# Kernel optimization log

Measured on AMD Instinct MI355X. Metric: run time of the kernel, lower is better.

Reference implementation:

```python
import jax, jax.numpy as jnp
import numpy as np

EPS = 1e-5
NEG_SLOPE = 0.2

def _layernorm(x, g, b):
    mu = x.mean(-1, keepdims=True)
    var = ((x - mu) ** 2).mean(-1, keepdims=True)
    return (x - mu) * jax.lax.rsqrt(var + EPS) * g + b

def _forward(h, edge_attr, rel_emb, W_l, b_l, W_r, b_r, W_e, att, bias, gate,
             g1, bt1, g2, bt2, Wf1, bf1, Wf2, bf2, edge_index, edge_type):
    N, F = h.shape
    R, H, C = att.shape
    HC = H * C
    E = edge_type.shape[0]
    De = edge_attr.shape[1]
    src, dst = edge_index[0], edge_index[1]

    # per-relation GATv2 linear projections: lin_l / lin_r  -> [N, R, H*C]
    xl = jnp.einsum('nf,rfh->nrh', h, W_l) + b_l
    xr = jnp.einsum('nf,rfh->nrh', h, W_r) + b_r
    # gather per edge using its own relation's weights
    xl_e = xl[src, edge_type]          # [E, HC]  (source, lin_l)
    xr_e = xr[dst, edge_type]          # [E, HC]  (dest,  lin_r)

    # edge features: lin_edge over concat([edge_attr, rel_emb[r]]) with per-relation weights
    e_feat = jnp.zeros((E, HC), dtype=h.dtype)
    for r in range(R):
        vr = edge_attr @ W_e[r, :De] + rel_emb[r] @ W_e[r, De:]  # [E,HC] + [HC]
        e_feat = jnp.where((edge_type == r)[:, None], vr, e_feat)

    # GATv2 attention score
    x = jax.nn.leaky_relu(xl_e + xr_e + e_feat, NEG_SLOPE).reshape(E, H, C)
    score = jnp.einsum('ehc,ehc->eh', x, att[edge_type])  # [E, H]

    # segment softmax per (destination node, relation)
    seg = dst * R + edge_type                              # [E]
    m = jax.lax.stop_gradient(jax.ops.segment_max(score, seg, num_segments=N * R))
    alpha = jnp.exp(score - m[seg])
    denom = jax.ops.segment_sum(alpha, seg, num_segments=N * R)
    alpha = alpha / denom[seg]                             # [E, H]

    # aggregate messages alpha * x_j (x_j = lin_l source features)
    msg = (xl_e.reshape(E, H, C) * alpha[..., None]).reshape(E, HC)
    agg = jax.ops.segment_sum(msg, seg, num_segments=N * R).reshape(N, R, H, C)
    h_rel = agg.mean(axis=2) + bias                        # concat=False -> head mean; [N, R, C]

    # learnable gated fusion over relations
    gw = jax.nn.softmax(gate)
    h_msg = jnp.einsum('r,nrc->nc', gw, h_rel)

    h1 = _layernorm(h + h_msg, g1, bt1)
    ffn = jax.nn.silu(h1 @ Wf1 + bf1) @ Wf2 + bf2
    return _layernorm(h1 + ffn, g2, bt2)


def setup_inputs() -> dict:
    key = jax.random.key(0)
    ks = jax.random.split(key, 16)
    N, F, E, De, Dr, R, H = 40000, 128, 150000, 16, 8, 4, 4
    C = F; HC = H * C; FFN = int(F * 2.0)
    s = 0.05
    return {
        'h': jax.random.normal(ks[0], (N, F), jnp.float32),
        'edge_index': jax.random.randint(ks[1], (2, E), 0, N),
        'edge_attr': jax.random.normal(ks[2], (E, De), jnp.float32),
        'edge_type': jax.random.randint(ks[3], (E,), 0, R),
        'rel_emb': jax.random.normal(ks[4], (R, Dr), jnp.float32) * s,
        'W_l': jax.random.normal(ks[5], (R, F, HC), jnp.float32) * s,
        'b_l': jnp.zeros((R, HC), jnp.float32),
        'W_r': jax.random.normal(ks[6], (R, F, HC), jnp.float32) * s,
        'b_r': jnp.zeros((R, HC), jnp.float32),
        'W_e': jax.random.normal(ks[7], (R, De + Dr, HC), jnp.float32) * s,
        'att': jax.random.normal(ks[8], (R, H, C), jnp.float32) * s,
        'bias': jnp.zeros((R, C), jnp.float32),
        'gate': jax.random.normal(ks[9], (R,), jnp.float32) * 0.5,
        'g1': jnp.ones((F,), jnp.float32), 'bt1': jnp.zeros((F,), jnp.float32),
        'g2': jnp.ones((F,), jnp.float32), 'bt2': jnp.zeros((F,), jnp.float32),
        'Wf1': jax.random.normal(ks[10], (F, FFN), jnp.float32) * s,
        'bf1': jnp.zeros((FFN,), jnp.float32),
        'Wf2': jax.random.normal(ks[11], (FFN, F), jnp.float32) * s,
        'bf2': jnp.zeros((F,), jnp.float32),
    }


def reference(h, edge_index, edge_attr, edge_type, rel_emb, W_l, b_l, W_r, b_r,
              W_e, att, bias, gate, g1, bt1, g2, bt2, Wf1, bf1, Wf2, bf2):
    return _forward(h, edge_attr, rel_emb, W_l, b_l, W_r, b_r, W_e, att, bias, gate,
                    g1, bt1, g2, bt2, Wf1, bf1, Wf2, bf2, edge_index, edge_type)
```

## Files before the change

kernel.cpp:

```cpp
#include <hip/hip_runtime.h>
#include <hip/hip_bf16.h>

#define NF   128
#define HCC  512
#define FFND 256
#define NEG  0.2f
#define EPSLN 1e-5f

typedef __attribute__((ext_vector_type(8))) short short8;
typedef __attribute__((ext_vector_type(4))) float f32x4;

__global__ void init_gw_kernel(const float* __restrict__ gate, float* __restrict__ gw) {
  if (threadIdx.x == 0 && blockIdx.x == 0) {
    float a = gate[0], b = gate[1], c = gate[2], d = gate[3];
    float m = fmaxf(fmaxf(a, b), fmaxf(c, d));
    float e0 = __expf(a - m), e1 = __expf(b - m), e2 = __expf(c - m), e3 = __expf(d - m);
    float s = e0 + e1 + e2 + e3;
    gw[0] = e0 / s; gw[1] = e1 / s; gw[2] = e2 / s; gw[3] = e3 / s;
  }
}

__global__ void init_all_kernel(float* __restrict__ denom, int* __restrict__ sorted,
                                int ndenom, int nsorted) {
  int i = blockIdx.x * 256 + threadIdx.x;
  if (i < ndenom)  denom[i] = 0.f;
  if (i < nsorted) sorted[i] = -1;
}

__global__ void init_hmsg_kernel(const float* __restrict__ gw, const float* __restrict__ bias,
                                 float* __restrict__ hmsg, int total) {
  int i = blockIdx.x * 256 + threadIdx.x;
  if (i < total) {
    int c = i & 127;
    hmsg[i] = gw[0]*bias[c] + gw[1]*bias[128+c] + gw[2]*bias[256+c] + gw[3]*bias[384+c];
  }
}

__global__ void transpose_bf16_kernel(const float* __restrict__ in, __hip_bfloat16* __restrict__ out,
                                      int rows, int cols, int total) {
  int i = blockIdx.x * 256 + threadIdx.x;
  if (i >= total) return;
  int per = rows * cols;
  int b = i / per, rem = i % per;
  int rr = rem / cols, cc = rem % cols;
  out[(size_t)b * per + (size_t)cc * rows + rr] = __float2bfloat16(in[i]);
}

__global__ void cvt_bf16_kernel(const float* __restrict__ in, __hip_bfloat16* __restrict__ out, int n) {
  int i4 = (blockIdx.x * 256 + threadIdx.x) * 4;
  if (i4 >= n) return;
  float4 v = *(const float4*)(in + i4);
  out[i4]     = __float2bfloat16(v.x);
  out[i4 + 1] = __float2bfloat16(v.y);
  out[i4 + 2] = __float2bfloat16(v.z);
  out[i4 + 3] = __float2bfloat16(v.w);
}

__global__ void prep_bias_kernel(const float* __restrict__ b_r, const float* __restrict__ rel_emb,
                                 const float* __restrict__ W_e, float* __restrict__ bias_comb) {
  int i = blockIdx.x * 256 + threadIdx.x;
  if (i >= 4 * 512) return;
  int col = i & 511, r = i >> 9;
  float v = b_r[i];
#pragma unroll
  for (int j = 0; j < 8; ++j)
    v += rel_emb[r * 8 + j] * W_e[(size_t)r * 24 * 512 + (size_t)(16 + j) * 512 + col];
  bias_comb[i] = v;
}

__global__ void blockhist_kernel(const int* __restrict__ etype, int* __restrict__ blockCnt, int E) {
  __shared__ int wcnt[4][4];
  int i = blockIdx.x * 256 + threadIdx.x;
  int rt = (i < E) ? etype[i] : -1;
  int wave = threadIdx.x >> 6, lane = threadIdx.x & 63;
#pragma unroll
  for (int r = 0; r < 4; ++r) {
    unsigned long long m = __ballot(rt == r);
    if (lane == 0) wcnt[wave][r] = __popcll(m);
  }
  __syncthreads();
  if (threadIdx.x < 4) {
    int r = threadIdx.x;
    blockCnt[blockIdx.x * 4 + r] = wcnt[0][r] + wcnt[1][r] + wcnt[2][r] + wcnt[3][r];
  }
}

__global__ void scan_kernel(const int* __restrict__ blockCnt, int* __restrict__ blockBase,
                            int* __restrict__ offs, int nBlocks) {
  __shared__ int lds[256];
  __shared__ int offs_s[5];
  __shared__ int tot_s[4];
  int t = threadIdx.x;
  int C = (nBlocks + 255) / 256;
  for (int r = 0; r < 4; ++r) {
    int s = 0;
    for (int b = t; b < nBlocks; b += 256) s += blockCnt[b * 4 + r];
    lds[t] = s;
    __syncthreads();
    for (int o = 128; o > 0; o >>= 1) {
      if (t < o) lds[t] += lds[t + o];
      __syncthreads();
    }
    if (t == 0) tot_s[r] = lds[0];
    __syncthreads();
  }
  if (t == 0) {
    int o = 0;
    offs_s[0] = 0;
    for (int r = 0; r < 4; ++r) { o += ((tot_s[r] + 63) >> 6) << 6; offs_s[r + 1] = o; }
    for (int r = 0; r < 5; ++r) offs[r] = offs_s[r];
  }
  __syncthreads();
  for (int r = 0; r < 4; ++r) {
    int b0 = t * C;
    int s = 0;
    for (int j = 0; j < C; ++j) {
      int b = b0 + j;
      if (b < nBlocks) s += blockCnt[b * 4 + r];
    }
    lds[t] = s;
    __syncthreads();
    int v = s;
    for (int o = 1; o < 256; o <<= 1) {
      int u = (t >= o) ? lds[t - o] : 0;
      __syncthreads();
      v += u;
      lds[t] = v;
      __syncthreads();
    }
    int run = offs_s[r] + (v - s);
    for (int j = 0; j < C; ++j) {
      int b = b0 + j;
      if (b < nBlocks) {
        blockBase[b * 4 + r] = run;
        run += blockCnt[b * 4 + r];
      }
    }
    __syncthreads();
  }
}

__global__ void scatter_kernel(const int* __restrict__ etype, const int* __restrict__ blockBase,
                               int* __restrict__ sorted, int E) {
  __shared__ int wcnt[4][4];
  int i = blockIdx.x * 256 + threadIdx.x;
  int rt = (i < E) ? etype[i] : -1;
  int wave = threadIdx.x >> 6, lane = threadIdx.x & 63;
  unsigned long long ltmask = (lane == 0) ? 0ull : (~0ull >> (64 - lane));
  int myrank = 0;
#pragma unroll
  for (int r = 0; r < 4; ++r) {
    unsigned long long m = __ballot(rt == r);
    if (lane == 0) wcnt[wave][r] = __popcll(m);
    if (rt == r) myrank = __popcll(m & ltmask);
  }
  __syncthreads();
  if (rt >= 0) {
    int wb = 0;
#pragma unroll
    for (int w = 0; w < 3; ++w) if (w < wave) wb += wcnt[w][rt];
    sorted[blockBase[blockIdx.x * 4 + rt] + wb + myrank] = i;
  }
}

__global__ __launch_bounds__(256) void mfma_gemm_kernel(
    const __hip_bfloat16* __restrict__ A,
    const __hip_bfloat16* __restrict__ Bt0, const float* __restrict__ bias0, void* __restrict__ out0,
    const __hip_bfloat16* __restrict__ Bt1, const float* __restrict__ bias1, void* __restrict__ out1,
    int M, int K, int Ncols, int act, int outBf)
{
  __shared__ __align__(16) short As[128 * 136];
  __shared__ __align__(16) short Bs[64 * 136];
  int z = blockIdx.z;
  const __hip_bfloat16* Bt = z ? Bt1 : Bt0;
  const float* bias = z ? bias1 : bias0;
  void* Cout = z ? out1 : out0;

  int tid = threadIdx.x;
  int rowBase = blockIdx.y * 128, colBase = blockIdx.x * 64;
  int wid = tid >> 6, lane = tid & 63;
  int m16 = lane & 15, q = lane >> 4;

  f32x4 acc[2][4];
#pragma unroll
  for (int mi = 0; mi < 2; ++mi)
#pragma unroll
    for (int ni = 0; ni < 4; ++ni) {
      acc[mi][ni][0] = 0.f; acc[mi][ni][1] = 0.f;
      acc[mi][ni][2] = 0.f; acc[mi][ni][3] = 0.f;
    }

#pragma unroll 1
  for (int kc = 0; kc < K; kc += 128) {
#pragma unroll
    for (int t = 0; t < 8; ++t) {
      int c = tid + t * 256;
      int row = c >> 4, kk = (c & 15) << 3;
      int grow = rowBase + row;
      short8 va;
      if (grow < M) va = *(const short8*)(const void*)(A + (size_t)grow * K + kc + kk);
      else { for (int zz = 0; zz < 8; ++zz) va[zz] = 0; }
      *(short8*)(void*)(As + row * 136 + kk) = va;
    }
#pragma unroll
    for (int t = 0; t < 4; ++t) {
      int c = tid + t * 256;
      int row = c >> 4, kk = (c & 15) << 3;
      *(short8*)(void*)(Bs + row * 136 + kk) =
        *(const short8*)(const void*)(Bt + (size_t)(colBase + row) * K + kc + kk);
    }
    __syncthreads();
#pragma unroll
    for (int ks = 0; ks < 4; ++ks) {
      int kof = (ks << 5) + (q << 3);
      short8 af[2], bfr[4];
#pragma unroll
      for (int mi = 0; mi < 2; ++mi)
        af[mi] = *(const short8*)(const void*)(As + (wid * 32 + mi * 16 + m16) * 136 + kof);
#pragma unroll
      for (int ni = 0; ni < 4; ++ni)
        bfr[ni] = *(const short8*)(const void*)(Bs + (ni * 16 + m16) * 136 + kof);
#pragma unroll
      for (int mi = 0; mi < 2; ++mi)
#pragma unroll
        for (int ni = 0; ni < 4; ++ni)
          acc[mi][ni] = __builtin_amdgcn_mfma_f32_16x16x32_bf16(af[mi], bfr[ni], acc[mi][ni], 0, 0, 0);
    }
    __syncthreads();
  }
#pragma unroll
  for (int mi = 0; mi < 2; ++mi)
#pragma unroll
    for (int ni = 0; ni < 4; ++ni) {
      int col = colBase + ni * 16 + m16;
      float bv = bias[col];
#pragma unroll
      for (int reg = 0; reg < 4; ++reg) {
        int row = rowBase + wid * 32 + mi * 16 + (q << 2) + reg;
        if (row < M) {
          float t = acc[mi][ni][reg] + bv;
          if (act) t = t / (1.f + __expf(-t));
          if (outBf) ((__hip_bfloat16*)Cout)[(size_t)row * Ncols + col] = __float2bfloat16(t);
          else       ((float*)Cout)[(size_t)row * Ncols + col] = t;
        }
      }
    }
}

__global__ __launch_bounds__(256) void score_kernel(
    const int* __restrict__ sorted, const int* __restrict__ offs, int r,
    const int* __restrict__ eidx, const float* __restrict__ eattr,
    const float* __restrict__ W_e, const float* __restrict__ att,
    const __hip_bfloat16* __restrict__ xlr, const __hip_bfloat16* __restrict__ xrr,
    float* __restrict__ alpha, float* __restrict__ denom, int N, int E)
{
  __shared__ float We_s[16 * 512];
  __shared__ float att_s[512];
  int tid = threadIdx.x;
#pragma unroll
  for (int t = 0; t < 32; ++t) {
    int idx = tid + (t << 8);
    We_s[idx] = W_e[((size_t)r * 24 + (idx >> 9)) * 512 + (idx & 511)];
  }
  att_s[tid]       = att[r * 512 + tid];
  att_s[tid + 256] = att[r * 512 + tid + 256];
  __syncthreads();

  int base = offs[r], end = offs[r + 1];
  int lane = tid & 63;
  int head = lane >> 4;
  int wave = (blockIdx.x << 2) + (tid >> 6);
  int nw = gridDim.x << 2;
  float4 atv0 = *(const float4*)(att_s + lane * 8);
  float4 atv1 = *(const float4*)(att_s + lane * 8 + 4);

  for (int i = base + wave; i < end; i += nw) {
    int eid = sorted[i];
    if (eid < 0) continue;
    int src = eidx[eid], dst = eidx[E + eid];
    float4 a0 = *(const float4*)(eattr + (size_t)eid * 16);
    float4 a1 = *(const float4*)(eattr + (size_t)eid * 16 + 4);
    float4 a2 = *(const float4*)(eattr + (size_t)eid * 16 + 8);
    float4 a3 = *(const float4*)(eattr + (size_t)eid * 16 + 12);
    float4 lv = *(const float4*)(const void*)(xlr + (size_t)src * 512 + lane * 8);
    float4 rv = *(const float4*)(const void*)(xrr + (size_t)dst * 512 + lane * 8);
    const unsigned* lw = (const unsigned*)&lv;
    const unsigned* rw = (const unsigned*)&rv;
    float x[8];
#pragma unroll
    for (int j = 0; j < 4; ++j) {
      x[2*j]   = __uint_as_float(lw[j] << 16)         + __uint_as_float(rw[j] << 16);
      x[2*j+1] = __uint_as_float(lw[j] & 0xffff0000u) + __uint_as_float(rw[j] & 0xffff0000u);
    }
    float aa[16] = {a0.x,a0.y,a0.z,a0.w, a1.x,a1.y,a1.z,a1.w,
                    a2.x,a2.y,a2.z,a2.w, a3.x,a3.y,a3.z,a3.w};
    float ef[8] = {0.f,0.f,0.f,0.f,0.f,0.f,0.f,0.f};
#pragma unroll
    for (int k = 0; k < 16; ++k) {
      float4 w0 = *(const float4*)(We_s + k * 512 + lane * 8);
      float4 w1 = *(const float4*)(We_s + k * 512 + lane * 8 + 4);
      ef[0] += aa[k]*w0.x; ef[1] += aa[k]*w0.y; ef[2] += aa[k]*w0.z; ef[3] += aa[k]*w0.w;
      ef[4] += aa[k]*w1.x; ef[5] += aa[k]*w1.y; ef[6] += aa[k]*w1.z; ef[7] += aa[k]*w1.w;
    }
    const float* at = (const float*)&atv0;
    float s = 0.f;
#pragma unroll
    for (int j = 0; j < 8; ++j) {
      float xv = x[j] + ef[j];
      xv = (xv > 0.f) ? xv : NEG * xv;
      s += xv * ((j < 4) ? at[j] : ((const float*)&atv1)[j - 4]);
    }
    s += __shfl_xor(s, 1);
    s += __shfl_xor(s, 2);
    s += __shfl_xor(s, 4);
    s += __shfl_xor(s, 8);
    if ((lane & 15) == 0) {
      float al = __expf(s);
      alpha[(size_t)eid * 4 + head] = al;
      atomicAdd(&denom[((size_t)r * N + dst) * 4 + head], al);
    }
  }
}

__global__ __launch_bounds__(256) void agg_kernel(
    const int* __restrict__ sorted, const int* __restrict__ offs, int r,
    const int* __restrict__ eidx, const float* __restrict__ alpha,
    const float* __restrict__ denom, const __hip_bfloat16* __restrict__ xlr,
    const float* __restrict__ gw, float* __restrict__ hmsg, int N, int E)
{
  int base = offs[r], end = offs[r + 1];
  float g = 0.25f * gw[r];
  int lane = threadIdx.x & 63;
  int wave = (blockIdx.x << 2) + (threadIdx.x >> 6);
  int nw = gridDim.x << 2;
  int col = lane * 2;
  for (int i = base + wave; i < end; i += nw) {
    int eid = sorted[i];
    if (eid < 0) continue;
    int src = eidx[eid], dst = eidx[E + eid];
    float4 al = *(const float4*)(alpha + (size_t)eid * 4);
    float4 dn = *(const float4*)(denom + ((size_t)r * N + dst) * 4);
    float coef[4] = {g * al.x / dn.x, g * al.y / dn.y, g * al.z / dn.z, g * al.w / dn.w};
    float s0 = 0.f, s1 = 0.f;
#pragma unroll
    for (int hh = 0; hh < 4; ++hh) {
      unsigned pw = *(const unsigned*)(const void*)(xlr + (size_t)src * 512 + hh * 128 + col);
      s0 += coef[hh] * __uint_as_float(pw << 16);
      s1 += coef[hh] * __uint_as_float(pw & 0xffff0000u);
    }
    atomicAdd(&hmsg[(size_t)dst * 128 + col],     s0);
    atomicAdd(&hmsg[(size_t)dst * 128 + col + 1], s1);
  }
}

__global__ __launch_bounds__(256) void ln_kernel(
    const float* __restrict__ X, const float* __restrict__ Y,
    const float* __restrict__ g, const float* __restrict__ b,
    float* __restrict__ out, __hip_bfloat16* __restrict__ outbf, int N)
{
  int w = (int)((blockIdx.x * (unsigned)blockDim.x + threadIdx.x) >> 6);
  int lane = threadIdx.x & 63;
  if (w >= N) return;
  int c = lane * 2;
  float2 xv = *(const float2*)(X + (size_t)w * 128 + c);
  float2 yv = *(const float2*)(Y + (size_t)w * 128 + c);
  float v0 = xv.x + yv.x, v1 = xv.y + yv.y;
  float s1 = v0 + v1, s2 = v0 * v0 + v1 * v1;
#pragma unroll
  for (int off = 1; off < 64; off <<= 1) {
    s1 += __shfl_xor(s1, off);
    s2 += __shfl_xor(s2, off);
  }
  float mu = s1 * (1.f / 128.f);
  float var = s2 * (1.f / 128.f) - mu * mu;
  float rstd = rsqrtf(var + EPSLN);
  float o0 = (v0 - mu) * rstd * g[c]     + b[c];
  float o1 = (v1 - mu) * rstd * g[c + 1] + b[c + 1];
  out[(size_t)w * 128 + c]     = o0;
  out[(size_t)w * 128 + c + 1] = o1;
  if (outbf) {
    outbf[(size_t)w * 128 + c]     = __float2bfloat16(o0);
    outbf[(size_t)w * 128 + c + 1] = __float2bfloat16(o1);
  }
}

extern "C" void kernel_launch(void* const* d_in, const int* in_sizes, int n_in,
                              void* d_out, int out_size, void* d_ws, size_t ws_size,
                              hipStream_t stream) {
  const float* h       = (const float*)d_in[0];
  const int*   eidx    = (const int*)d_in[1];
  const float* eattr   = (const float*)d_in[2];
  const int*   etype   = (const int*)d_in[3];
  const float* rel_emb = (const float*)d_in[4];
  const float* W_l     = (const float*)d_in[5];
  const float* b_l     = (const float*)d_in[6];
  const float* W_r     = (const float*)d_in[7];
  const float* b_r     = (const float*)d_in[8];
  const float* W_e     = (const float*)d_in[9];
  const float* att     = (const float*)d_in[10];
  const float* bias    = (const float*)d_in[11];
  const float* gate    = (const float*)d_in[12];
  const float* g1      = (const float*)d_in[13];
  const float* bt1     = (const float*)d_in[14];
  const float* g2      = (const float*)d_in[15];
  const float* bt2     = (const float*)d_in[16];
  const float* Wf1     = (const float*)d_in[17];
  const float* bf1     = (const float*)d_in[18];
  const float* Wf2     = (const float*)d_in[19];
  const float* bf2     = (const float*)d_in[20];

  const int N = in_sizes[0] / NF;
  const int E = in_sizes[3];
  const int nTiles = (E + 4 * 63 + 63) / 64;
  const int sortedN = nTiles * 64;
  const int Mtiles = (N + 127) / 128;
  const int histBlocks = (E + 255) / 256;

  char* ws = (char*)d_ws;
  size_t off = 0;
  auto carve = [&](size_t bytes) -> void* {
    void* p = ws + off;
    off = (off + bytes + 255) & ~(size_t)255;
    return p;
  };
  __hip_bfloat16* xl_r  = (__hip_bfloat16*)carve((size_t)N * 512 * 2);
  __hip_bfloat16* xr_r  = (__hip_bfloat16*)carve((size_t)N * 512 * 2);
  __hip_bfloat16* hbf   = (__hip_bfloat16*)carve((size_t)N * 128 * 2);
  __hip_bfloat16* Wlt   = (__hip_bfloat16*)carve((size_t)4 * 512 * 128 * 2);
  __hip_bfloat16* Wrt   = (__hip_bfloat16*)carve((size_t)4 * 512 * 128 * 2);
  __hip_bfloat16* Wf1t  = (__hip_bfloat16*)carve((size_t)256 * 128 * 2);
  __hip_bfloat16* Wf2t  = (__hip_bfloat16*)carve((size_t)128 * 256 * 2);
  float*    bias_c = (float*)carve((size_t)4 * 512 * 4);
  float*    alpha  = (float*)carve((size_t)E * 4 * 4);
  float*    denom  = (float*)carve((size_t)4 * N * 4 * 4);
  float*    hmsg   = (float*)carve((size_t)N * 128 * 4);
  int*      sorted = (int*)carve((size_t)sortedN * 4);
  int*      blockCnt  = (int*)carve((size_t)histBlocks * 4 * 4);
  int*      blockBase = (int*)carve((size_t)histBlocks * 4 * 4);
  int*      offsb  = (int*)carve(64);
  float*    gw     = (float*)carve(256);
  float*          h1   = (float*)(ws + 0);
  __hip_bfloat16* h1bf = (__hip_bfloat16*)(ws + (size_t)N * 128 * 4);
  __hip_bfloat16* uffn = (__hip_bfloat16*)(ws + (size_t)N * 128 * 6);
  float*          yffn = (float*)(ws + (size_t)N * 128 * 6 + (size_t)N * 256 * 2);
  float*          out  = (float*)d_out;

  init_gw_kernel<<<1, 64, 0, stream>>>(gate, gw);
  {
    int ndenom = 4 * N * 4;
    int mx = (ndenom > sortedN) ? ndenom : sortedN;
    init_all_kernel<<<(mx + 255) / 256, 256, 0, stream>>>(denom, sorted, ndenom, sortedN);
  }
  init_hmsg_kernel<<<(N * 128 + 255) / 256, 256, 0, stream>>>(gw, bias, hmsg, N * 128);
  cvt_bf16_kernel<<<(N * 128 / 4 + 255) / 256, 256, 0, stream>>>(h, hbf, N * 128);
  transpose_bf16_kernel<<<(4 * 128 * 512 + 255) / 256, 256, 0, stream>>>(W_l, Wlt, 128, 512, 4 * 128 * 512);
  transpose_bf16_kernel<<<(4 * 128 * 512 + 255) / 256, 256, 0, stream>>>(W_r, Wrt, 128, 512, 4 * 128 * 512);
  transpose_bf16_kernel<<<(128 * 256 + 255) / 256, 256, 0, stream>>>(Wf1, Wf1t, 128, 256, 128 * 256);
  transpose_bf16_kernel<<<(256 * 128 + 255) / 256, 256, 0, stream>>>(Wf2, Wf2t, 256, 128, 256 * 128);
  prep_bias_kernel<<<(4 * 512 + 255) / 256, 256, 0, stream>>>(b_r, rel_emb, W_e, bias_c);
  blockhist_kernel<<<histBlocks, 256, 0, stream>>>(etype, blockCnt, E);
  scan_kernel<<<1, 256, 0, stream>>>(blockCnt, blockBase, offsb, histBlocks);
  scatter_kernel<<<histBlocks, 256, 0, stream>>>(etype, blockBase, sorted, E);

  for (int r = 0; r < 4; ++r) {
    mfma_gemm_kernel<<<dim3(HCC / 64, Mtiles, 2), 256, 0, stream>>>(
        hbf,
        Wlt + (size_t)r * 512 * 128, b_l + r * 512, (void*)xl_r,
        Wrt + (size_t)r * 512 * 128, bias_c + r * 512, (void*)xr_r,
        N, 128, HCC, 0, 1);
    score_kernel<<<1024, 256, 0, stream>>>(sorted, offsb, r, eidx, eattr, W_e, att,
                                           xl_r, xr_r, alpha, denom, N, E);
    agg_kernel<<<1024, 256, 0, stream>>>(sorted, offsb, r, eidx, alpha, denom,
                                         xl_r, gw, hmsg, N, E);
  }

  ln_kernel<<<(N + 3) / 4, 256, 0, stream>>>(h, hmsg, g1, bt1, h1, h1bf, N);
  mfma_gemm_kernel<<<dim3(FFND / 64, Mtiles, 1), 256, 0, stream>>>(
      h1bf, Wf1t, bf1, (void*)uffn, Wf1t, bf1, (void*)uffn, N, 128, FFND, 1, 1);
  mfma_gemm_kernel<<<dim3(NF / 64, Mtiles, 1), 256, 0, stream>>>(
      uffn, Wf2t, bf2, (void*)yffn, Wf2t, bf2, (void*)yffn, N, 256, NF, 0, 0);
  ln_kernel<<<(N + 3) / 4, 256, 0, stream>>>(h1, yffn, g2, bt2, out, nullptr, N);
}
```

Baseline: 746.4 us.

## Keep A tile resident in registers and loop over all column blocks per block

Adds a projection GEMM kernel where each block loads its 128-row A tile once into registers and iterates over all column blocks of both projections (xl and xr), double-buffering the weight tiles in shared memory. This replaces the grid with one block per row tile, removing redundant A reloads across column blocks and z-slices. It is also used for the first FFN GEMM with SiLU. The cost is far fewer blocks (Mtiles only), so less parallelism and occupancy on the GPU, plus a serial column loop per block.

```diff
diff --git a/kernel.cpp b/kernel.cpp
--- a/kernel.cpp
+++ b/kernel.cpp
@@ -163,19 +163,123 @@
   }
 }
 
+__global__ __launch_bounds__(256) void proj_multi_kernel(
+    const __hip_bfloat16* __restrict__ A,
+    const __hip_bfloat16* __restrict__ Bt0, const float* __restrict__ bias0,
+    __hip_bfloat16* __restrict__ out0,
+    const __hip_bfloat16* __restrict__ Bt1, const float* __restrict__ bias1,
+    __hip_bfloat16* __restrict__ out1,
+    int M, int nch, int sides, int act)
+{
+  __shared__ __align__(16) short As[128 * 136];
+  __shared__ __align__(16) short Bs[2][64 * 136];
+  int tid = threadIdx.x;
+  int rowBase = blockIdx.x * 128;
+  int wid = tid >> 6, lane = tid & 63;
+  int m16 = lane & 15, q = lane >> 4;
+  int total = nch * sides;
+
+#pragma unroll
+  for (int t = 0; t < 8; ++t) {
+    int c = tid + t * 256;
+    int row = c >> 4, kk = (c & 15) << 3;
+    int grow = rowBase + row;
+    short8 va;
+    if (grow < M) va = *(const short8*)(const void*)(A + (size_t)grow * 128 + kk);
+    else { for (int zz = 0; zz < 8; ++zz) va[zz] = 0; }
+    *(short8*)(void*)(As + row * 136 + kk) = va;
+  }
+  __syncthreads();
+  short8 af[4][2];
+#pragma unroll
+  for (int ks = 0; ks < 4; ++ks)
+#pragma unroll
+    for (int mi = 0; mi < 2; ++mi)
+      af[ks][mi] = *(const short8*)(const void*)(As + (wid * 32 + mi * 16 + m16) * 136 + (ks << 5) + (q << 3));
+
+  {
+    const __hip_bfloat16* Bt = Bt0;
+#pragma unroll
+    for (int t = 0; t < 4; ++t) {
+      int c = tid + t * 256;
+      int row = c >> 4, kk = (c & 15) << 3;
+      *(short8*)(void*)(Bs[0] + row * 136 + kk) =
+        *(const short8*)(const void*)(Bt + (size_t)row * 128 + kk);
+    }
+  }
+  __syncthreads();
+
+  int p = 0;
+  for (int cb = 0; cb < total; ++cb) {
+    int side = cb >= nch;
+    int colBase = (side ? (cb - nch) : cb) * 64;
+    f32x4 acc[2][4];
+#pragma unroll
+    for (int mi = 0; mi < 2; ++mi)
+#pragma unroll
+      for (int ni = 0; ni < 4; ++ni) {
+        acc[mi][ni][0] = 0.f; acc[mi][ni][1] = 0.f;
+        acc[mi][ni][2] = 0.f; acc[mi][ni][3] = 0.f;
+      }
+#pragma unroll
+    for (int ks = 0; ks < 4; ++ks) {
+      int kof = (ks << 5) + (q << 3);
+      short8 bfr[4];
+#pragma unroll
+      for (int ni = 0; ni < 4; ++ni)
+        bfr[ni] = *(const short8*)(const void*)(Bs[p] + (ni * 16 + m16) * 136 + kof);
+#pragma unroll
+      for (int mi = 0; mi < 2; ++mi)
+#pragma unroll
+        for (int ni = 0; ni < 4; ++ni)
+          acc[mi][ni] = __builtin_amdgcn_mfma_f32_16x16x32_bf16(af[ks][mi], bfr[ni], acc[mi][ni], 0, 0, 0);
+    }
+    if (cb + 1 < total) {
+      int nc = cb + 1;
+      int nside = nc >= nch;
+      int ncol = (nside ? (nc - nch) : nc) * 64;
+      const __hip_bfloat16* Bt = nside ? Bt1 : Bt0;
+#pragma unroll
+      for (int t = 0; t < 4; ++t) {
+        int c = tid + t * 256;
+        int row = c >> 4, kk = (c & 15) << 3;
+        *(short8*)(void*)(Bs[p ^ 1] + row * 136 + kk) =
+          *(const short8*)(const void*)(Bt + (size_t)(ncol + row) * 128 + kk);
+      }
+    }
+    {
+      const float* bias = side ? bias1 : bias0;
+      __hip_bfloat16* out = side ? out1 : out0;
+      int ldc = nch * 64;
+#pragma unroll
+      for (int mi = 0; mi < 2; ++mi)
+#pragma unroll
+        for (int ni = 0; ni < 4; ++ni) {
+          int col = colBase + ni * 16 + m16;
+          float bv = bias[col];
+#pragma unroll
+          for (int reg = 0; reg < 4; ++reg) {
+            int row = rowBase + wid * 32 + mi * 16 + (q << 2) + reg;
+            if (row < M) {
+              float t = acc[mi][ni][reg] + bv;
+              if (act) t = t / (1.f + __expf(-t));
+              out[(size_t)row * ldc + col] = __float2bfloat16(t);
+            }
+          }
+        }
+    }
+    __syncthreads();
+    p ^= 1;
+  }
+}
+
 __global__ __launch_bounds__(256) void mfma_gemm_kernel(
     const __hip_bfloat16* __restrict__ A,
-    const __hip_bfloat16* __restrict__ Bt0, const float* __restrict__ bias0, void* __restrict__ out0,
-    const __hip_bfloat16* __restrict__ Bt1, const float* __restrict__ bias1, void* __restrict__ out1,
-    int M, int K, int Ncols, int act, int outBf)
+    const __hip_bfloat16* __restrict__ Bt, const float* __restrict__ bias,
+    float* __restrict__ Cout, int M, int K, int Ncols)
 {
   __shared__ __align__(16) short As[128 * 136];
   __shared__ __align__(16) short Bs[64 * 136];
-  int z = blockIdx.z;
-  const __hip_bfloat16* Bt = z ? Bt1 : Bt0;
-  const float* bias = z ? bias1 : bias0;
-  void* Cout = z ? out1 : out0;
-
   int tid = threadIdx.x;
   int rowBase = blockIdx.y * 128, colBase = blockIdx.x * 64;
   int wid = tid >> 6, lane = tid & 63;
@@ -237,12 +341,7 @@
 #pragma unroll
       for (int reg = 0; reg < 4; ++reg) {
         int row = rowBase + wid * 32 + mi * 16 + (q << 2) + reg;
-        if (row < M) {
-          float t = acc[mi][ni][reg] + bv;
-          if (act) t = t / (1.f + __expf(-t));
-          if (outBf) ((__hip_bfloat16*)Cout)[(size_t)row * Ncols + col] = __float2bfloat16(t);
-          else       ((float*)Cout)[(size_t)row * Ncols + col] = t;
-        }
+        if (row < M) Cout[(size_t)row * Ncols + col] = acc[mi][ni][reg] + bv;
       }
     }
 }
@@ -463,11 +562,11 @@
   scatter_kernel<<<histBlocks, 256, 0, stream>>>(etype, blockBase, sorted, E);
 
   for (int r = 0; r < 4; ++r) {
-    mfma_gemm_kernel<<<dim3(HCC / 64, Mtiles, 2), 256, 0, stream>>>(
+    proj_multi_kernel<<<Mtiles, 256, 0, stream>>>(
         hbf,
-        Wlt + (size_t)r * 512 * 128, b_l + r * 512, (void*)xl_r,
-        Wrt + (size_t)r * 512 * 128, bias_c + r * 512, (void*)xr_r,
-        N, 128, HCC, 0, 1);
+        Wlt + (size_t)r * 512 * 128, b_l + r * 512, xl_r,
+        Wrt + (size_t)r * 512 * 128, bias_c + r * 512, xr_r,
+        N, 8, 2, 0);
     score_kernel<<<1024, 256, 0, stream>>>(sorted, offsb, r, eidx, eattr, W_e, att,
                                            xl_r, xr_r, alpha, denom, N, E);
     agg_kernel<<<1024, 256, 0, stream>>>(sorted, offsb, r, eidx, alpha, denom,
@@ -475,9 +574,9 @@
   }
 
   ln_kernel<<<(N + 3) / 4, 256, 0, stream>>>(h, hmsg, g1, bt1, h1, h1bf, N);
-  mfma_gemm_kernel<<<dim3(FFND / 64, Mtiles, 1), 256, 0, stream>>>(
-      h1bf, Wf1t, bf1, (void*)uffn, Wf1t, bf1, (void*)uffn, N, 128, FFND, 1, 1);
-  mfma_gemm_kernel<<<dim3(NF / 64, Mtiles, 1), 256, 0, stream>>>(
-      uffn, Wf2t, bf2, (void*)yffn, Wf2t, bf2, (void*)yffn, N, 256, NF, 0, 0);
+  proj_multi_kernel<<<Mtiles, 256, 0, stream>>>(
+      h1bf, Wf1t, bf1, uffn, Wf1t, bf1, uffn, N, 4, 1, 1);
+  mfma_gemm_kernel<<<dim3(NF / 64, Mtiles), 256, 0, stream>>>(
+      uffn, Wf2t, bf2, yffn, N, 256, NF);
   ln_kernel<<<(N + 3) / 4, 256, 0, stream>>>(h1, yffn, g2, bt2, out, nullptr, N);
 }
```

Result: slower. 768.7 us (+3.0%).
